# Performance work log

Measured on AMD Instinct MI355X. Metric: run time of the kernel, lower is better.

Reference implementation:

```python
import jax, jax.numpy as jnp
import numpy as np

B, L, D = 4096, 128, 60  # states, padded buffer length, word+char+tag dim
HIDDEN, OUT = 200, 3


def setup_inputs() -> dict:
    key = jax.random.key(0)
    ks = jax.random.split(key, 8)
    buffer = jax.random.normal(ks[0], (B, L, D), dtype=jnp.float32)
    # buffer_index in [1, L-4] so buffer_index+3 stays in range (shift still legal region varies)
    buffer_index = jax.random.randint(ks[1], (B,), 0, 124)
    stack_indexes = jax.random.randint(ks[2], (B, 3), 0, L)
    stack_len = jax.random.randint(ks[3], (B,), 0, 12)
    W1 = jax.random.normal(ks[4], (6 * D, HIDDEN), dtype=jnp.float32) * 0.05
    b1 = jnp.zeros((HIDDEN,), dtype=jnp.float32)
    W2 = jax.random.normal(ks[5], (HIDDEN, OUT), dtype=jnp.float32) * 0.05
    b2 = jnp.zeros((OUT,), dtype=jnp.float32)
    return {"buffer": buffer, "W1": W1, "b1": b1, "W2": W2, "b2": b2,
            "buffer_index": buffer_index, "stack_indexes": stack_indexes,
            "stack_len": stack_len}


def reference(buffer, W1, b1, W2, b2, buffer_index, stack_indexes, stack_len):
    Bn, Ln, Dn = buffer.shape
    # gather 3 contiguous buffer slots per state: buffer[b, bi:bi+3]
    buf_idx = buffer_index[:, None] + jnp.arange(3)           # [B, 3]
    buffers = jnp.take_along_axis(buffer, buf_idx[:, :, None], axis=1).reshape(Bn, -1)
    # gather top-3 stack slots per state
    stacks = jnp.take_along_axis(buffer, stack_indexes[:, :, None], axis=1).reshape(Bn, -1)
    X = jnp.concatenate([buffers, stacks], axis=1)            # [B, 6*D]
    hid = jax.nn.relu(X @ W1 + b1)
    out = hid @ W2 + b2                                       # [B, 3]
    # legal action mask
    legal = jnp.stack([
        jnp.where(buffer_index + 3 >= Ln, 0.0, 1.0),  # shift legal iff buffer not exhausted
        jnp.where(stack_len <= 3, 0.0, 1.0),          # left-arc
        jnp.where(stack_len <= 4, 0.0, 1.0),          # right-arc
    ], axis=1).astype(jnp.float32)
    return out, legal
```

## Files before the change

kernel.cpp:

```cpp
#include <hip/hip_runtime.h>


#define Bq    4096
#define Lq    128
#define Dq    60
#define HIDq  200
#define ONUM  3
#define KTN   12
#define MB    16
#define NTHR  512
#define SLABW 196

typedef short bf16x8 __attribute__((ext_vector_type(8)));
typedef float f32x4  __attribute__((ext_vector_type(4)));

__device__ __forceinline__ unsigned int rhu(float f) {
    union { float f; unsigned int u; } x; x.f = f;
    return x.u + 0x8000u;
}
__device__ __forceinline__ int pack2(float lo, float hi) {
    return (int)__builtin_amdgcn_perm(rhu(hi), rhu(lo), 0x07060302u);
}

__global__ __launch_bounds__(NTHR, 1) void parser_fused(
    const float* __restrict__ buffer,
    const float* __restrict__ W1,
    const float* __restrict__ b1,
    const float* __restrict__ W2,
    const float* __restrict__ b2,
    const int*   __restrict__ buffer_index,
    const int*   __restrict__ stack_indexes,
    const int*   __restrict__ stack_len,
    float*       __restrict__ out)
{
    __shared__ unsigned short Afrag[KTN * 64 * 8];
    __shared__ unsigned int   wbuf[8][16 * SLABW];
    __shared__ float          psum[8][MB][ONUM];

    const int t  = threadIdx.x;
    const int w  = t >> 6;
    const int l  = t & 63;
    const int s0 = blockIdx.x * MB;

    const bool hasB1 = (w < 5);

    #define STAGE_SLAB(ntile)                                                      \
    {                                                                              \
        _Pragma("unroll")                                                          \
        for (int it = 0; it < 12; ++it) {                                          \
            int j = it * 64 + l;                                                   \
            if (it < 11 || l < 16) {                                  \
                int k2 = j >> 2, nq = j & 3;                                       \
                int nb = (ntile) * 16 + nq * 4;                                    \
                float4 v0 = {0.f,0.f,0.f,0.f}, v1 = {0.f,0.f,0.f,0.f};             \
                if (nb < HIDq) {                                                   \
                    const float* p = W1 + (size_t)(2 * k2) * HIDq + nb;            \
                    v0 = *(const float4*)p;                                        \
                    v1 = *(const float4*)(p + HIDq);                               \
                }                                                                  \
                wbuf[w][(nq*4+0)*SLABW + k2] = (unsigned)pack2(v0.x, v1.x);        \
                wbuf[w][(nq*4+1)*SLABW + k2] = (unsigned)pack2(v0.y, v1.y);        \
                wbuf[w][(nq*4+2)*SLABW + k2] = (unsigned)pack2(v0.z, v1.z);        \
                wbuf[w][(nq*4+3)*SLABW + k2] = (unsigned)pack2(v0.w, v1.w);        \
            }                                                                      \
        }                                                                          \
    }

    #pragma unroll
    for (int z = 0; z < 3; ++z) {
        int idx = z * 64 + l;
        wbuf[w][(idx / 12) * SLABW + 180 + (idx % 12)] = 0u;
    }

    STAGE_SLAB(w)

    bf16x8 B0[KTN], B1[KTN];
    #pragma unroll
    for (int kt = 0; kt < KTN; ++kt)
        B0[kt] = *((const bf16x8*)&wbuf[w][(l & 15) * SLABW + kt * 16 + ((l >> 4) << 2)]);

    if (hasB1) {
        STAGE_SLAB(8 + w)
        #pragma unroll
        for (int kt = 0; kt < KTN; ++kt)
            B1[kt] = *((const bf16x8*)&wbuf[w][(l & 15) * SLABW + kt * 16 + ((l >> 4) << 2)]);
    }
    #undef STAGE_SLAB

    const int  n0   = w * 16 + (l & 15);
    const int  n1   = (8 + w) * 16 + (l & 15);
    const bool n1ok = n1 < HIDq;
    float bb0 = b1[n0];
    float w20 = W2[n0 * ONUM + 0], w21 = W2[n0 * ONUM + 1], w22 = W2[n0 * ONUM + 2];
    float bb1 = 0.f, w23 = 0.f, w24 = 0.f, w25 = 0.f;
    if (hasB1 && n1ok) {
        bb1 = b1[n1];
        w23 = W2[n1 * ONUM + 0]; w24 = W2[n1 * ONUM + 1]; w25 = W2[n1 * ONUM + 2];
    }

    #define GATHER_JOB(i)                                                        \
    {                                                                            \
        int s = (i) / 90, r = (i) % 90, seg = r / 15, f = r % 15;                \
        int row = (seg < 3) ? (buffer_index[s0 + s] + seg)                       \
                            : stack_indexes[(s0 + s) * 3 + (seg - 3)];           \
        float4 v = ((const float4*)(buffer + ((size_t)(s0 + s) * Lq + row) * Dq))[f]; \
        int k0   = seg * 60 + f * 4;                                             \
        int kt   = k0 >> 5;                                                      \
        int lane = s + (((k0 & 31) >> 3) << 4);                                  \
        uint2 pk;                                                                \
        pk.x = (unsigned)pack2(v.x, v.y);                                        \
        pk.y = (unsigned)pack2(v.z, v.w);                                        \
        *((uint2*)&Afrag[(size_t)(kt * 64 + lane) * 8 + (k0 & 7)]) = pk;         \
    }
    GATHER_JOB(t)
    GATHER_JOB(t + 512)
    if (t < 416) GATHER_JOB(t + 1024)
    #undef GATHER_JOB

    if (t < 48) {
        f32x4 z = {0.f, 0.f, 0.f, 0.f};
        *((f32x4*)&Afrag[(size_t)(11 * 64 + 16 + t) * 8]) = z;
    }

    if (t < MB * ONUM) {
        int s = t / ONUM, o = t % ONUM;
        int bi = buffer_index[s0 + s];
        int sl = stack_len[s0 + s];
        float lg;
        if (o == 0)      lg = (bi + 3 >= Lq) ? 0.f : 1.f;
        else if (o == 1) lg = (sl <= 3)      ? 0.f : 1.f;
        else             lg = (sl <= 4)      ? 0.f : 1.f;
        out[(size_t)Bq * ONUM + (size_t)(s0 + s) * ONUM + o] = lg;
    }
    __syncthreads();

    f32x4 acc0 = {}, acc1 = {};
    #pragma unroll
    for (int kt = 0; kt < KTN; ++kt) {
        bf16x8 a = *((const bf16x8*)&Afrag[(size_t)(kt * 64 + l) * 8]);
        acc0 = __builtin_amdgcn_mfma_f32_16x16x32_bf16(a, B0[kt], acc0, 0, 0, 0);
        if (hasB1)
            acc1 = __builtin_amdgcn_mfma_f32_16x16x32_bf16(a, B1[kt], acc1, 0, 0, 0);
    }

    float p[ONUM][4];
    #pragma unroll
    for (int o = 0; o < ONUM; ++o)
        #pragma unroll
        for (int r = 0; r < 4; ++r) p[o][r] = 0.f;

    #pragma unroll
    for (int r = 0; r < 4; ++r) {
        float h = acc0[r] + bb0; h = h > 0.f ? h : 0.f;
        p[0][r] = fmaf(h, w20, p[0][r]);
        p[1][r] = fmaf(h, w21, p[1][r]);
        p[2][r] = fmaf(h, w22, p[2][r]);
    }
    if (hasB1) {
        #pragma unroll
        for (int r = 0; r < 4; ++r) {
            float h = acc1[r] + bb1; h = h > 0.f ? h : 0.f;
            p[0][r] = fmaf(h, w23, p[0][r]);
            p[1][r] = fmaf(h, w24, p[1][r]);
            p[2][r] = fmaf(h, w25, p[2][r]);
        }
    }

    #pragma unroll
    for (int d = 1; d < 16; d <<= 1) {
        #pragma unroll
        for (int o = 0; o < ONUM; ++o)
            #pragma unroll
            for (int r = 0; r < 4; ++r)
                p[o][r] += __shfl_xor(p[o][r], d, 64);
    }
    if ((l & 15) == 0) {
        #pragma unroll
        for (int r = 0; r < 4; ++r) {
            int s = ((l >> 4) << 2) + r;
            #pragma unroll
            for (int o = 0; o < ONUM; ++o) psum[w][s][o] = p[o][r];
        }
    }
    __syncthreads();

    if (t < MB * ONUM) {
        int s = t / ONUM, o = t % ONUM;
        float v = b2[o];
        #pragma unroll
        for (int w8 = 0; w8 < 8; ++w8) v += psum[w8][s][o];
        out[(size_t)(s0 + s) * ONUM + o] = v;
    }
}

extern "C" void kernel_launch(void* const* d_in, const int* in_sizes, int n_in,
                              void* d_out, int out_size, void* d_ws, size_t ws_size,
                              hipStream_t stream) {
    const float* buffer        = (const float*)d_in[0];
    const float* W1            = (const float*)d_in[1];
    const float* b1            = (const float*)d_in[2];
    const float* W2            = (const float*)d_in[3];
    const float* b2            = (const float*)d_in[4];
    const int*   buffer_index  = (const int*)d_in[5];
    const int*   stack_indexes = (const int*)d_in[6];
    const int*   stack_len     = (const int*)d_in[7];
    float*       out           = (float*)d_out;

    parser_fused<<<Bq / MB, NTHR, 0, stream>>>(
        buffer, W1, b1, W2, b2, buffer_index, stack_indexes, stack_len, out);
}
```

Before: 14.61 us.

## Reorder loads to overlap W1 slab staging with buffer gathers

Restructures the prologue so the gather indices, the first W1 slab loads, the activation gathers and the second W1 slab loads are all issued early into registers, and the LDS packing happens afterwards. The aim is to put more global loads in flight at once and hide their latency, instead of serialising load, pack and read per slab. The cost is much higher register pressure (48 extra float4 values), which could cause spills, although with one block per CU occupancy is already low.

Result: slower. 15.52 us (+6.3%).

```diff
diff --git a/kernel.cpp b/kernel.cpp
--- a/kernel.cpp
+++ b/kernel.cpp
@@ -41,51 +41,34 @@
     const int w  = t >> 6;
     const int l  = t & 63;
     const int s0 = blockIdx.x * MB;
-
     const bool hasB1 = (w < 5);
 
-    #define STAGE_SLAB(ntile)                                                      \
-    {                                                                              \
-        _Pragma("unroll")                                                          \
-        for (int it = 0; it < 12; ++it) {                                          \
-            int j = it * 64 + l;                                                   \
-            if (it < 11 || l < 16) {                                  \
-                int k2 = j >> 2, nq = j & 3;                                       \
-                int nb = (ntile) * 16 + nq * 4;                                    \
-                float4 v0 = {0.f,0.f,0.f,0.f}, v1 = {0.f,0.f,0.f,0.f};             \
-                if (nb < HIDq) {                                                   \
-                    const float* p = W1 + (size_t)(2 * k2) * HIDq + nb;            \
-                    v0 = *(const float4*)p;                                        \
-                    v1 = *(const float4*)(p + HIDq);                               \
-                }                                                                  \
-                wbuf[w][(nq*4+0)*SLABW + k2] = (unsigned)pack2(v0.x, v1.x);        \
-                wbuf[w][(nq*4+1)*SLABW + k2] = (unsigned)pack2(v0.y, v1.y);        \
-                wbuf[w][(nq*4+2)*SLABW + k2] = (unsigned)pack2(v0.z, v1.z);        \
-                wbuf[w][(nq*4+3)*SLABW + k2] = (unsigned)pack2(v0.w, v1.w);        \
-            }                                                                      \
-        }                                                                          \
-    }
-
-    #pragma unroll
-    for (int z = 0; z < 3; ++z) {
-        int idx = z * 64 + l;
-        wbuf[w][(idx / 12) * SLABW + 180 + (idx % 12)] = 0u;
-    }
-
-    STAGE_SLAB(w)
-
-    bf16x8 B0[KTN], B1[KTN];
-    #pragma unroll
-    for (int kt = 0; kt < KTN; ++kt)
-        B0[kt] = *((const bf16x8*)&wbuf[w][(l & 15) * SLABW + kt * 16 + ((l >> 4) << 2)]);
-
-    if (hasB1) {
-        STAGE_SLAB(8 + w)
-        #pragma unroll
-        for (int kt = 0; kt < KTN; ++kt)
-            B1[kt] = *((const bf16x8*)&wbuf[w][(l & 15) * SLABW + kt * 16 + ((l >> 4) << 2)]);
-    }
-    #undef STAGE_SLAB
+    int g_s[3], g_row[3], g_k0[3];
+    #pragma unroll
+    for (int m = 0; m < 3; ++m) {
+        int i = t + m * 512;
+        bool ok = (m < 2) || (t < 416);
+        if (ok) {
+            int s = i / 90, r = i % 90, seg = r / 15, f = r % 15;
+            g_s[m]  = s;
+            g_k0[m] = seg * 60 + f * 4;
+            g_row[m] = (seg < 3) ? (buffer_index[s0 + s] + seg)
+                                 : stack_indexes[(s0 + s) * 3 + (seg - 3)];
+        } else { g_s[m] = 0; g_row[m] = 0; g_k0[m] = 0; }
+    }
+
+    float4 s0a[12], s0b[12];
+    #pragma unroll
+    for (int it = 0; it < 12; ++it) {
+        int j = it * 64 + l;
+        if (it < 11 || l < 16) {
+            int k2 = j >> 2, nq = j & 3;
+            int nb = w * 16 + nq * 4;
+            const float* p = W1 + (size_t)(2 * k2) * HIDq + nb;
+            s0a[it] = *(const float4*)p;
+            s0b[it] = *(const float4*)(p + HIDq);
+        }
+    }
 
     const int  n0   = w * 16 + (l & 15);
     const int  n1   = (8 + w) * 16 + (l & 15);
@@ -98,30 +81,76 @@
         w23 = W2[n1 * ONUM + 0]; w24 = W2[n1 * ONUM + 1]; w25 = W2[n1 * ONUM + 2];
     }
 
-    #define GATHER_JOB(i)                                                        \
-    {                                                                            \
-        int s = (i) / 90, r = (i) % 90, seg = r / 15, f = r % 15;                \
-        int row = (seg < 3) ? (buffer_index[s0 + s] + seg)                       \
-                            : stack_indexes[(s0 + s) * 3 + (seg - 3)];           \
-        float4 v = ((const float4*)(buffer + ((size_t)(s0 + s) * Lq + row) * Dq))[f]; \
-        int k0   = seg * 60 + f * 4;                                             \
-        int kt   = k0 >> 5;                                                      \
-        int lane = s + (((k0 & 31) >> 3) << 4);                                  \
-        uint2 pk;                                                                \
-        pk.x = (unsigned)pack2(v.x, v.y);                                        \
-        pk.y = (unsigned)pack2(v.z, v.w);                                        \
-        *((uint2*)&Afrag[(size_t)(kt * 64 + lane) * 8 + (k0 & 7)]) = pk;         \
-    }
-    GATHER_JOB(t)
-    GATHER_JOB(t + 512)
-    if (t < 416) GATHER_JOB(t + 1024)
-    #undef GATHER_JOB
-
+    float4 gv[3];
+    #pragma unroll
+    for (int m = 0; m < 3; ++m) {
+        bool ok = (m < 2) || (t < 416);
+        if (ok) {
+            int off = g_k0[m] % 60;
+            gv[m] = *(const float4*)(buffer +
+                     ((size_t)(s0 + g_s[m]) * Lq + g_row[m]) * Dq + off);
+        }
+    }
+
+    #pragma unroll
+    for (int z = 0; z < 3; ++z) {
+        int idx = z * 64 + l;
+        wbuf[w][(idx / 12) * SLABW + 180 + (idx % 12)] = 0u;
+    }
+
+    #pragma unroll
+    for (int it = 0; it < 12; ++it) {
+        int j = it * 64 + l;
+        if (it < 11 || l < 16) {
+            int k2 = j >> 2, nq = j & 3;
+            wbuf[w][(nq * 4 + 0) * SLABW + k2] = (unsigned)pack2(s0a[it].x, s0b[it].x);
+            wbuf[w][(nq * 4 + 1) * SLABW + k2] = (unsigned)pack2(s0a[it].y, s0b[it].y);
+            wbuf[w][(nq * 4 + 2) * SLABW + k2] = (unsigned)pack2(s0a[it].z, s0b[it].z);
+            wbuf[w][(nq * 4 + 3) * SLABW + k2] = (unsigned)pack2(s0a[it].w, s0b[it].w);
+        }
+    }
+
+    float4 s1a[12], s1b[12];
+    if (hasB1) {
+        #pragma unroll
+        for (int it = 0; it < 12; ++it) {
+            int j = it * 64 + l;
+            if (it < 11 || l < 16) {
+                int k2 = j >> 2, nq = j & 3;
+                int nb = 128 + w * 16 + nq * 4;
+                if (nb < HIDq) {
+                    const float* p = W1 + (size_t)(2 * k2) * HIDq + nb;
+                    s1a[it] = *(const float4*)p;
+                    s1b[it] = *(const float4*)(p + HIDq);
+                } else {
+                    s1a[it] = (float4){0.f, 0.f, 0.f, 0.f};
+                    s1b[it] = (float4){0.f, 0.f, 0.f, 0.f};
+                }
+            }
+        }
+    }
+
+    bf16x8 B0[KTN], B1[KTN];
+    #pragma unroll
+    for (int kt = 0; kt < KTN; ++kt)
+        B0[kt] = *((const bf16x8*)&wbuf[w][(l & 15) * SLABW + kt * 16 + ((l >> 4) << 2)]);
+
+    #pragma unroll
+    for (int m = 0; m < 3; ++m) {
+        bool ok = (m < 2) || (t < 416);
+        if (ok) {
+            int kt   = g_k0[m] >> 5;
+            int lane = g_s[m] + (((g_k0[m] & 31) >> 3) << 4);
+            uint2 pk;
+            pk.x = (unsigned)pack2(gv[m].x, gv[m].y);
+            pk.y = (unsigned)pack2(gv[m].z, gv[m].w);
+            *((uint2*)&Afrag[(size_t)(kt * 64 + lane) * 8 + (g_k0[m] & 7)]) = pk;
+        }
+    }
     if (t < 48) {
         f32x4 z = {0.f, 0.f, 0.f, 0.f};
         *((f32x4*)&Afrag[(size_t)(11 * 64 + 16 + t) * 8]) = z;
     }
-
     if (t < MB * ONUM) {
         int s = t / ONUM, o = t % ONUM;
         int bi = buffer_index[s0 + s];
@@ -132,6 +161,24 @@
         else             lg = (sl <= 4)      ? 0.f : 1.f;
         out[(size_t)Bq * ONUM + (size_t)(s0 + s) * ONUM + o] = lg;
     }
+
+    if (hasB1) {
+        #pragma unroll
+        for (int it = 0; it < 12; ++it) {
+            int j = it * 64 + l;
+            if (it < 11 || l < 16) {
+                int k2 = j >> 2, nq = j & 3;
+                wbuf[w][(nq * 4 + 0) * SLABW + k2] = (unsigned)pack2(s1a[it].x, s1b[it].x);
+                wbuf[w][(nq * 4 + 1) * SLABW + k2] = (unsigned)pack2(s1a[it].y, s1b[it].y);
+                wbuf[w][(nq * 4 + 2) * SLABW + k2] = (unsigned)pack2(s1a[it].z, s1b[it].z);
+                wbuf[w][(nq * 4 + 3) * SLABW + k2] = (unsigned)pack2(s1a[it].w, s1b[it].w);
+            }
+        }
+        #pragma unroll
+        for (int kt = 0; kt < KTN; ++kt)
+            B1[kt] = *((const bf16x8*)&wbuf[w][(l & 15) * SLABW + kt * 16 + ((l >> 4) << 2)]);
+    }
+
     __syncthreads();
 
     f32x4 acc0 = {}, acc1 = {};
```
